# Kernel tuning notes

Measured on AMD Instinct MI355X. Metric: run time of the kernel, lower is better.

Reference implementation:

```python
import jax, jax.numpy as jnp
import numpy as np

N = 50000
IN_CH = 256
HEADS = 8
OUT_CH = 32
E = 800000


def setup_inputs() -> dict:
    key = jax.random.key(0)
    k1, k2, k3, k4, k5 = jax.random.split(key, 5)
    x = jax.random.normal(k1, (N, IN_CH), dtype=jnp.float32)
    edge_index = jax.random.randint(k2, (2, E), 0, N, dtype=jnp.int64)
    # torch Linear(in, heads*out, bias=False): weight [heads*out, in]
    W = jax.random.normal(k3, (HEADS * OUT_CH, IN_CH), dtype=jnp.float32) / np.sqrt(IN_CH)
    # xavier_uniform over (1, heads, out)
    bound = float(np.sqrt(6.0 / (HEADS + OUT_CH)))
    attn_l = jax.random.uniform(k4, (1, HEADS, OUT_CH), minval=-bound, maxval=bound, dtype=jnp.float32)
    attn_r = jax.random.uniform(k5, (1, HEADS, OUT_CH), minval=-bound, maxval=bound, dtype=jnp.float32)
    return {"x": x, "edge_index": edge_index, "W": W, "attn_l": attn_l, "attn_r": attn_r}


def reference(x, edge_index, W, attn_l, attn_r):
    num_nodes = x.shape[0]
    # node-level projection: [N, H, C]
    xp = (x @ W.T).reshape(num_nodes, HEADS, OUT_CH).astype(jnp.float32)
    # add self loops
    loops = jnp.arange(num_nodes, dtype=edge_index.dtype)
    src = jnp.concatenate([edge_index[0], loops])
    dst = jnp.concatenate([edge_index[1], loops])
    # edge attention logits per head: [Etot, H]
    alpha_l = (xp * attn_l).sum(-1)[src]
    alpha_r = (xp * attn_r).sum(-1)[dst]
    alpha = jax.nn.leaky_relu(alpha_l + alpha_r, negative_slope=0.2)
    # global per-head max subtraction (as in the original), then scatter softmax over dst
    alpha = jnp.exp(alpha - alpha.max(axis=0, keepdims=True))
    alpha_sum = jax.ops.segment_sum(alpha, dst, num_segments=num_nodes)  # [N, H]
    alpha = alpha / jnp.maximum(alpha_sum[dst], 1e-6)
    # weighted aggregation: scatter-add alpha * x_src to dst, all heads at once
    msgs = alpha[:, :, None] * xp[src]  # [Etot, H, C]
    out = jax.ops.segment_sum(msgs, dst, num_segments=num_nodes)  # [N, H, C]
    return out.reshape(num_nodes, HEADS * OUT_CH)
```

## Files before the change

kernel.cpp:

```cpp
#include <hip/hip_runtime.h>
#include <math.h>

#define IN_CH   256
#define HEADS   8
#define OUT_CH  32
#define CAP     64

typedef __attribute__((ext_vector_type(8))) short s16x8;
typedef __attribute__((ext_vector_type(4))) float f32x4;
typedef __attribute__((address_space(1))) const unsigned int gu32;
typedef __attribute__((address_space(3))) unsigned int lu32;

__device__ inline short f2bf(float f) {
  unsigned u = __builtin_bit_cast(unsigned, f);
  u += 0x7fffu + ((u >> 16) & 1u);
  return (short)(u >> 16);
}

__global__ __launch_bounds__(256) void prep(
    const float* __restrict__ W, short* __restrict__ Wq,
    int* __restrict__ cnt, int* __restrict__ csrs, int n, int cnt_blocks) {
  const int b = blockIdx.x;
  const int tid = threadIdx.x;
  if (b < 32) {
    const int g = b * 256 + tid;
    const int oc = g & 255, s = (g >> 8) & 7, t = g >> 11;
    const float* sp = W + oc * IN_CH + t * 64 + s * 8;
    float4 lo = *(const float4*)sp;
    float4 hi = *(const float4*)(sp + 4);
    s16x8 v;
    v[0] = f2bf(lo.x); v[1] = f2bf(lo.y); v[2] = f2bf(lo.z); v[3] = f2bf(lo.w);
    v[4] = f2bf(hi.x); v[5] = f2bf(hi.y); v[6] = f2bf(hi.z); v[7] = f2bf(hi.w);
    *(s16x8*)&Wq[g * 8] = v;
  } else if (b < 32 + cnt_blocks) {
    const int i = ((b - 32) * 256 + tid) * 4;
    *(int4*)(cnt + i) = make_int4(1, 1, 1, 1);
  } else {
    const int d = (b - 32 - cnt_blocks) * 256 + tid;
    if (d < n) csrs[(size_t)d * CAP] = d;
  }
}

__device__ inline void fill_edges(const int* __restrict__ src_idx,
                                  const int* __restrict__ dst_idx,
                                  int* __restrict__ cnt,
                                  int* __restrict__ csrs, int E,
                                  int tg, int tot) {
  for (int e = tg * 4; e < E; e += tot * 4) {
    int ss[4], dd[4];
    if ((E & 3) == 0 && e + 3 < E) {
      const int4 a = *(const int4*)(src_idx + e);
      const int4 b = *(const int4*)(dst_idx + e);
      ss[0] = a.x; ss[1] = a.y; ss[2] = a.z; ss[3] = a.w;
      dd[0] = b.x; dd[1] = b.y; dd[2] = b.z; dd[3] = b.w;
    } else {
#pragma unroll
      for (int i = 0; i < 4; ++i) {
        if (e + i < E) { ss[i] = src_idx[e + i]; dd[i] = dst_idx[e + i]; }
        else dd[i] = -1;
      }
    }
#pragma unroll
    for (int i = 0; i < 4; ++i) {
      if (dd[i] >= 0) {
        const int p = atomicAdd(&cnt[dd[i]], 1);
        if (p < CAP) csrs[dd[i] * CAP + p] = ss[i];
      }
    }
  }
}

__global__ __launch_bounds__(256) void gemm_fill(
    const float* __restrict__ x, const short* __restrict__ Wq,
    const float* __restrict__ attn_l, const float* __restrict__ attn_r,
    short* __restrict__ xpb, float* __restrict__ al, float* __restrict__ ar,
    const int* __restrict__ src_idx, const int* __restrict__ dst_idx,
    int* __restrict__ cnt, int* __restrict__ csrs, int E, int n) {
  const int tid = threadIdx.x;
  const int tg  = (int)blockIdx.x * 256 + tid;
  const int tot = (int)gridDim.x * 256;
  const bool fill_first = (blockIdx.x & 1) == 0;

  if (fill_first) fill_edges(src_idx, dst_idx, cnt, csrs, E, tg, tot);

  __shared__ short Ws[8 * 256 * 8];
  __shared__ short Xs[8 * 64 * 8];
  const int wave = tid >> 6;
  const int lane = tid & 63;
  const int nrow = lane & 15;
  const int kq   = lane >> 4;
  const int node0 = blockIdx.x * 64;

  f32x4 acc[4][4];
#pragma unroll
  for (int i = 0; i < 4; ++i)
#pragma unroll
    for (int j = 0; j < 4; ++j) acc[i][j] = (f32x4){0.f, 0.f, 0.f, 0.f};

  for (int t = 0; t < 4; ++t) {
    __syncthreads();
#pragma unroll
    for (int s = 0; s < 8; ++s) {
      const short* gp = Wq + ((t * 8 + s) * 256 + tid) * 8;
      __builtin_amdgcn_global_load_lds(
          (gu32*)gp, (lu32*)&Ws[(s * 256 + wave * 64) * 8], 16, 0, 0);
    }
    const int k0 = t * 64;
#pragma unroll
    for (int p = 0; p < 2; ++p) {
      const int c = p * 256 + tid;
      const int row = c >> 3, o = c & 7;
      int grow = node0 + row;
      if (grow >= n) grow = n - 1;
      const float* xr = x + (size_t)grow * IN_CH + k0 + o * 8;
      float4 lo = *(const float4*)xr;
      float4 hi = *(const float4*)(xr + 4);
      s16x8 v;
      v[0] = f2bf(lo.x); v[1] = f2bf(lo.y); v[2] = f2bf(lo.z); v[3] = f2bf(lo.w);
      v[4] = f2bf(hi.x); v[5] = f2bf(hi.y); v[6] = f2bf(hi.z); v[7] = f2bf(hi.w);
      *(s16x8*)&Xs[(o * 64 + row) * 8] = v;
    }
    __syncthreads();
#pragma unroll
    for (int kk = 0; kk < 2; ++kk) {
      const int o = kk * 4 + kq;
      s16x8 af[4], bf[4];
#pragma unroll
      for (int i = 0; i < 4; ++i)
        af[i] = *(const s16x8*)&Ws[(o * 256 + wave * 64 + i * 16 + nrow) * 8];
#pragma unroll
      for (int j = 0; j < 4; ++j)
        bf[j] = *(const s16x8*)&Xs[(o * 64 + j * 16 + nrow) * 8];
#pragma unroll
      for (int i = 0; i < 4; ++i)
#pragma unroll
        for (int j = 0; j < 4; ++j)
          acc[i][j] = __builtin_amdgcn_mfma_f32_16x16x32_bf16(
              af[i], bf[j], acc[i][j], 0, 0, 0);
    }
  }

  float pl[4][2] = {}, pr[4][2] = {};
#pragma unroll
  for (int i = 0; i < 4; ++i) {
    const int oc = wave * 64 + i * 16 + kq * 4;
    const float4 la = *(const float4*)(attn_l + oc);
    const float4 ra = *(const float4*)(attn_r + oc);
    const int hh = i >> 1;
#pragma unroll
    for (int j = 0; j < 4; ++j) {
      const int node = node0 + j * 16 + nrow;
      ushort4 st;
      st.x = (unsigned short)f2bf(acc[i][j][0]);
      st.y = (unsigned short)f2bf(acc[i][j][1]);
      st.z = (unsigned short)f2bf(acc[i][j][2]);
      st.w = (unsigned short)f2bf(acc[i][j][3]);
      if (node < n) *(ushort4*)(xpb + (size_t)node * IN_CH + oc) = st;
      pl[j][hh] += acc[i][j][0] * la.x + acc[i][j][1] * la.y +
                   acc[i][j][2] * la.z + acc[i][j][3] * la.w;
      pr[j][hh] += acc[i][j][0] * ra.x + acc[i][j][1] * ra.y +
                   acc[i][j][2] * ra.z + acc[i][j][3] * ra.w;
    }
  }
#pragma unroll
  for (int j = 0; j < 4; ++j)
#pragma unroll
    for (int hh = 0; hh < 2; ++hh) {
      float vl = pl[j][hh], vr = pr[j][hh];
      vl += __shfl_xor(vl, 16); vl += __shfl_xor(vl, 32);
      vr += __shfl_xor(vr, 16); vr += __shfl_xor(vr, 32);
      const int node = node0 + j * 16 + nrow;
      if (kq == 0 && node < n) {
        al[node * HEADS + wave * 2 + hh] = vl;
        ar[node * HEADS + wave * 2 + hh] = vr;
      }
    }

  if (!fill_first) fill_edges(src_idx, dst_idx, cnt, csrs, E, tg, tot);
}

__device__ inline void acc8(float w, const s16x8& u, float* acc) {
  const unsigned* p = (const unsigned*)&u;
#pragma unroll
  for (int j = 0; j < 4; ++j) {
    const unsigned v = p[j];
    const float flo = __builtin_bit_cast(float, v << 16);
    const float fhi = __builtin_bit_cast(float, v & 0xFFFF0000u);
    acc[2 * j]     = fmaf(w, flo, acc[2 * j]);
    acc[2 * j + 1] = fmaf(w, fhi, acc[2 * j + 1]);
  }
}

__global__ __launch_bounds__(256) void gat_gather(
    const int* __restrict__ csrs, const int* __restrict__ cntp,
    const short* __restrict__ xpb, const float* __restrict__ al,
    const float* __restrict__ ar, float* __restrict__ out, int n) {
  const int gid = blockIdx.x * blockDim.x + threadIdx.x;
  const int d = gid >> 6;
  if (d >= n) return;
  const int lane = gid & 63;
  const int half = lane >> 5;
  const int cl = lane & 31;
  const int h = cl >> 2;
  const int start = d * CAP;
  int cnt = cntp[d];
  if (cnt > CAP) cnt = CAP;
  const float ard = ar[d * HEADS + h];

  float acc[8] = {0.f, 0.f, 0.f, 0.f, 0.f, 0.f, 0.f, 0.f};
  float denom = 0.f;
  for (int jb = 0; jb < cnt; jb += 8) {
    const int base = jb + half * 4;
    const int4 q = *(const int4*)(csrs + start + base);
    const int* qp = (const int*)&q;
    int s[4];
#pragma unroll
    for (int i = 0; i < 4; ++i) s[i] = (base + i < cnt) ? qp[i] : d;
    s16x8 u[4];
#pragma unroll
    for (int i = 0; i < 4; ++i)
      u[i] = *(const s16x8*)(xpb + (size_t)s[i] * IN_CH + cl * 8);
    float w[4];
#pragma unroll
    for (int i = 0; i < 4; ++i) {
      float a = al[s[i] * HEADS + h] + ard;
      a = a > 0.f ? a : 0.2f * a;
      w[i] = (base + i < cnt) ? __expf(a) : 0.f;
      denom += w[i];
    }
#pragma unroll
    for (int i = 0; i < 4; ++i) acc8(w[i], u[i], acc);
  }
  denom += __shfl_xor(denom, 32);
#pragma unroll
  for (int k = 0; k < 8; ++k) acc[k] += __shfl_xor(acc[k], 32);
  if (half == 0) {
    const float inv = 1.f / fmaxf(denom, 1e-6f);
    f32x4 v0 = {acc[0] * inv, acc[1] * inv, acc[2] * inv, acc[3] * inv};
    f32x4 v1 = {acc[4] * inv, acc[5] * inv, acc[6] * inv, acc[7] * inv};
    float* op = out + (size_t)d * IN_CH + cl * 8;
    __builtin_nontemporal_store(v0, (f32x4*)op);
    __builtin_nontemporal_store(v1, (f32x4*)(op + 4));
  }
}

extern "C" void kernel_launch(void* const* d_in, const int* in_sizes, int n_in,
                              void* d_out, int out_size, void* d_ws,
                              size_t ws_size, hipStream_t stream) {
  const float* x      = (const float*)d_in[0];
  const int*   ei     = (const int*)d_in[1];
  const float* W      = (const float*)d_in[2];
  const float* attn_l = (const float*)d_in[3];
  const float* attn_r = (const float*)d_in[4];
  float* out = (float*)d_out;

  const int n = in_sizes[0] / IN_CH;
  const int E = in_sizes[1] / 2;

  short* xpb  = (short*)d_ws;
  short* Wq   = xpb + (size_t)n * IN_CH;
  float* al   = (float*)(Wq + IN_CH * IN_CH);
  float* ar   = al + (size_t)n * HEADS;
  int*   cnt  = (int*)(ar + (size_t)n * HEADS);
  const int cnt_blocks = (n + 1023) / 1024;
  int*   csrs = cnt + (size_t)cnt_blocks * 1024;

  const int seed_blocks = (n + 255) / 256;
  prep<<<32 + cnt_blocks + seed_blocks, 256, 0, stream>>>(
      W, Wq, cnt, csrs, n, cnt_blocks);

  const int gemm_blocks = (n + 63) / 64;
  gemm_fill<<<gemm_blocks, 256, 0, stream>>>(
      x, Wq, attn_l, attn_r, xpb, al, ar, ei, ei + E, cnt, csrs, E, n);

  const long long g_threads = (long long)n * 64;
  gat_gather<<<(int)((g_threads + 255) / 256), 256, 0, stream>>>(
      csrs, cnt, xpb, al, ar, out, n);
}
```

Baseline: 226.7 us.

## Double-buffer neighbor gathers and preload CSR indices via wave shuffles

New measurement: 223.1 us. No clear change (-1.6%).

```diff
diff --git a/kernel.cpp b/kernel.cpp
--- a/kernel.cpp
+++ b/kernel.cpp
@@ -8,6 +8,7 @@
 
 typedef __attribute__((ext_vector_type(8))) short s16x8;
 typedef __attribute__((ext_vector_type(4))) float f32x4;
+typedef __attribute__((ext_vector_type(2))) float f32x2;
 typedef __attribute__((address_space(1))) const unsigned int gu32;
 typedef __attribute__((address_space(3))) unsigned int lu32;
 
@@ -179,18 +180,6 @@
   if (!fill_first) fill_edges(src_idx, dst_idx, cnt, csrs, E, tg, tot);
 }
 
-__device__ inline void acc8(float w, const s16x8& u, float* acc) {
-  const unsigned* p = (const unsigned*)&u;
-#pragma unroll
-  for (int j = 0; j < 4; ++j) {
-    const unsigned v = p[j];
-    const float flo = __builtin_bit_cast(float, v << 16);
-    const float fhi = __builtin_bit_cast(float, v & 0xFFFF0000u);
-    acc[2 * j]     = fmaf(w, flo, acc[2 * j]);
-    acc[2 * j + 1] = fmaf(w, fhi, acc[2 * j + 1]);
-  }
-}
-
 __global__ __launch_bounds__(256) void gat_gather(
     const int* __restrict__ csrs, const int* __restrict__ cntp,
     const short* __restrict__ xpb, const float* __restrict__ al,
@@ -202,42 +191,77 @@
   const int half = lane >> 5;
   const int cl = lane & 31;
   const int h = cl >> 2;
-  const int start = d * CAP;
   int cnt = cntp[d];
   if (cnt > CAP) cnt = CAP;
   const float ard = ar[d * HEADS + h];
 
-  float acc[8] = {0.f, 0.f, 0.f, 0.f, 0.f, 0.f, 0.f, 0.f};
+  int myidx = d;
+  if (lane < cnt) myidx = csrs[d * CAP + lane];
+
+  f32x2 acc2[4] = {{0.f, 0.f}, {0.f, 0.f}, {0.f, 0.f}, {0.f, 0.f}};
   float denom = 0.f;
-  for (int jb = 0; jb < cnt; jb += 8) {
-    const int base = jb + half * 4;
-    const int4 q = *(const int4*)(csrs + start + base);
-    const int* qp = (const int*)&q;
-    int s[4];
-#pragma unroll
-    for (int i = 0; i < 4; ++i) s[i] = (base + i < cnt) ? qp[i] : d;
-    s16x8 u[4];
-#pragma unroll
-    for (int i = 0; i < 4; ++i)
-      u[i] = *(const s16x8*)(xpb + (size_t)s[i] * IN_CH + cl * 8);
-    float w[4];
-#pragma unroll
-    for (int i = 0; i < 4; ++i) {
-      float a = al[s[i] * HEADS + h] + ard;
-      a = a > 0.f ? a : 0.2f * a;
-      w[i] = (base + i < cnt) ? __expf(a) : 0.f;
-      denom += w[i];
-    }
-#pragma unroll
-    for (int i = 0; i < 4; ++i) acc8(w[i], u[i], acc);
-  }
+
+  s16x8 u0[4], u1[4];
+  float a0[4], a1[4];
+
+#define ISSUE(JB, U, A)                                                   \
+  {                                                                       \
+    const int base_ = (JB) + half * 4;                                    \
+    int s_[4];                                                            \
+    _Pragma("unroll")                                                     \
+    for (int i_ = 0; i_ < 4; ++i_) s_[i_] = __shfl(myidx, base_ + i_);    \
+    _Pragma("unroll")                                                     \
+    for (int i_ = 0; i_ < 4; ++i_)                                        \
+      U[i_] = *(const s16x8*)(xpb + (size_t)s_[i_] * IN_CH + cl * 8);     \
+    _Pragma("unroll")                                                     \
+    for (int i_ = 0; i_ < 4; ++i_) A[i_] = al[s_[i_] * HEADS + h];        \
+  }
+
+#define CONSUME(JB, U, A)                                                 \
+  {                                                                       \
+    _Pragma("unroll")                                                     \
+    for (int i_ = 0; i_ < 4; ++i_) {                                      \
+      float aa_ = A[i_] + ard;                                            \
+      aa_ = aa_ > 0.f ? aa_ : 0.2f * aa_;                                 \
+      const float w_ =                                                    \
+          ((JB) + half * 4 + i_ < cnt) ? __expf(aa_) : 0.f;               \
+      denom += w_;                                                        \
+      const f32x2 wv_ = {w_, w_};                                         \
+      const unsigned* p_ = (const unsigned*)&U[i_];                       \
+      _Pragma("unroll")                                                   \
+      for (int j_ = 0; j_ < 4; ++j_) {                                    \
+        const unsigned v_ = p_[j_];                                       \
+        f32x2 t_;                                                         \
+        t_[0] = __builtin_bit_cast(float, v_ << 16);                      \
+        t_[1] = __builtin_bit_cast(float, v_ & 0xFFFF0000u);              \
+        acc2[j_] = wv_ * t_ + acc2[j_];                                   \
+      }                                                                   \
+    }                                                                     \
+  }
+
+  ISSUE(0, u0, a0);
+  int jb = 0;
+  while (true) {
+    if (jb + 8 < cnt) ISSUE(jb + 8, u1, a1);
+    CONSUME(jb, u0, a0);
+    jb += 8;
+    if (jb >= cnt) break;
+    if (jb + 8 < cnt) ISSUE(jb + 8, u0, a0);
+    CONSUME(jb, u1, a1);
+    jb += 8;
+    if (jb >= cnt) break;
+  }
+#undef ISSUE
+#undef CONSUME
+
+  float* accf = (float*)acc2;
   denom += __shfl_xor(denom, 32);
 #pragma unroll
-  for (int k = 0; k < 8; ++k) acc[k] += __shfl_xor(acc[k], 32);
+  for (int k = 0; k < 8; ++k) accf[k] += __shfl_xor(accf[k], 32);
   if (half == 0) {
     const float inv = 1.f / fmaxf(denom, 1e-6f);
-    f32x4 v0 = {acc[0] * inv, acc[1] * inv, acc[2] * inv, acc[3] * inv};
-    f32x4 v1 = {acc[4] * inv, acc[5] * inv, acc[6] * inv, acc[7] * inv};
+    f32x4 v0 = {accf[0] * inv, accf[1] * inv, accf[2] * inv, accf[3] * inv};
+    f32x4 v1 = {accf[4] * inv, accf[5] * inv, accf[6] * inv, accf[7] * inv};
     float* op = out + (size_t)d * IN_CH + cl * 8;
     __builtin_nontemporal_store(v0, (f32x4*)op);
     __builtin_nontemporal_store(v1, (f32x4*)(op + 4));
```
